# Kernel tuning notes

Measured on AMD Instinct MI355X. Metric: run time of the kernel, lower is better.

The kernel has to match this reference:

```python
import jax, jax.numpy as jnp
import numpy as np

N_NODES = 10000
N_EDGES = 640000
IN_FEATS = 256
H_FEATS = 128
NUM_CLASSES = 64


def _kaiming(key, shape):
    fan_in = shape[1]
    std = np.sqrt(2.0 / fan_in)
    return jax.random.normal(key, shape, dtype=jnp.float32) * std


def setup_inputs() -> dict:
    key = jax.random.key(0)
    ks = jax.random.split(key, 10)
    x = jax.random.normal(ks[0], (N_NODES, IN_FEATS), dtype=jnp.float32)
    edge_index = jax.random.randint(ks[1], (2, N_EDGES), 0, N_NODES, dtype=jnp.int64)
    return {
        "x": x,
        "edge_index": edge_index,
        "W_lin": _kaiming(ks[2], (H_FEATS, IN_FEATS)),
        "b_lin": jnp.zeros((H_FEATS,), jnp.float32),
        "Wl1": _kaiming(ks[3], (H_FEATS, H_FEATS)),
        "bl1": jnp.zeros((H_FEATS,), jnp.float32),
        "Wr1": _kaiming(ks[4], (H_FEATS, H_FEATS)),
        "Wl2": _kaiming(ks[5], (H_FEATS, H_FEATS)),
        "bl2": jnp.zeros((H_FEATS,), jnp.float32),
        "Wr2": _kaiming(ks[6], (H_FEATS, H_FEATS)),
        "W_cls": _kaiming(ks[7], (NUM_CLASSES, H_FEATS)),
    }


def _sage_conv(x, src, dst, Wl, bl, Wr, n_nodes):
    # PyG SAGEConv (mean aggr): out = lin_l(mean_{j->i} x_j) + lin_r(x_i)
    msg = x[src]                                    # [E, H] gather
    agg = jax.ops.segment_sum(msg, dst, num_segments=n_nodes)  # [N, H]
    deg = jax.ops.segment_sum(jnp.ones((src.shape[0],), x.dtype), dst,
                              num_segments=n_nodes)            # [N]
    mean = agg / jnp.maximum(deg, 1.0)[:, None]
    return mean @ Wl.T + bl + x @ Wr.T


def reference(x, edge_index, W_lin, b_lin, Wl1, bl1, Wr1, Wl2, bl2, Wr2, W_cls):
    src, dst = edge_index[0], edge_index[1]
    n = x.shape[0]
    h = jax.nn.relu(x @ W_lin.T + b_lin)            # input projection + relu
    h = _sage_conv(h, src, dst, Wl1, bl1, Wr1, n)   # sage1 (no relu: linear is truthy)
    h = _sage_conv(h, src, dst, Wl2, bl2, Wr2, n)   # sage2
    h = jax.nn.relu(h)
    return h @ W_cls.T                              # weight.mm(x.t()).t()
```

## Files before the change

kernel.cpp:

```cpp
#include <hip/hip_runtime.h>

#define NN 10000
#define HF 128
#define INF_ 256
#define CLS 64
#define CAP 128
#define RT  (NN / 16)

typedef __attribute__((ext_vector_type(8))) short short8;
typedef __attribute__((ext_vector_type(4))) float f32x4;

__device__ __forceinline__ unsigned short f2bf(float f) {
    unsigned u = __builtin_bit_cast(unsigned, f);
    u = (u + 0x7fffu + ((u >> 16) & 1u)) >> 16;
    return (unsigned short)u;
}
__device__ __forceinline__ float bfbits2f(unsigned u) {
    u <<= 16;
    return __builtin_bit_cast(float, u);
}


template <int K, int NC>
__device__ __forceinline__
void mfma_cols(int row_tile, int col0,
               const unsigned short* __restrict__ A,
               const unsigned short* __restrict__ W, f32x4* acc) {
    int lane = threadIdx.x & 63;
    int m = lane & 15, quad = lane >> 4;
    const short8* ap = (const short8*)(A + (size_t)(row_tile * 16 + m) * K + quad * 8);
    const short8* bp[NC];
#pragma unroll
    for (int c = 0; c < NC; ++c)
        bp[c] = (const short8*)(W + (size_t)(col0 + c * 16 + m) * K + quad * 8);
#pragma unroll
    for (int k0 = 0; k0 < K; k0 += 32) {
        int ki = k0 >> 3;
        short8 a = ap[ki];
#pragma unroll
        for (int c = 0; c < NC; ++c)
            acc[c] = __builtin_amdgcn_mfma_f32_16x16x32_bf16(a, bp[c][ki], acc[c], 0, 0, 0);
    }
}

template <int NC, bool OUT_BF16, bool RELU_OUT, bool HAS_BIAS, bool HAS_TMP>
__device__ __forceinline__
void epilogue_n(int row_tile, int col0, int N, const float* __restrict__ bias,
                const float* __restrict__ tmp, f32x4* acc, void* __restrict__ out) {
    int lane = threadIdx.x & 63;
    int m = lane & 15, quad = lane >> 4;
#pragma unroll
    for (int c = 0; c < NC; ++c) {
        int colg = col0 + c * 16 + m;
        float bv = HAS_BIAS ? bias[colg] : 0.f;
#pragma unroll
        for (int r = 0; r < 4; ++r) {
            int rowg = row_tile * 16 + quad * 4 + r;
            float v = acc[c][r] + bv;
            if (HAS_TMP) v += tmp[(size_t)rowg * N + colg];
            if (RELU_OUT) v = fmaxf(v, 0.f);
            if (OUT_BF16) ((unsigned short*)out)[(size_t)rowg * N + colg] = f2bf(v);
            else          ((float*)out)[(size_t)rowg * N + colg] = v;
        }
    }
}

__device__ __forceinline__ short8 pack8(float4 a, float4 b) {
    short8 r;
    r[0] = (short)f2bf(a.x); r[1] = (short)f2bf(a.y);
    r[2] = (short)f2bf(a.z); r[3] = (short)f2bf(a.w);
    r[4] = (short)f2bf(b.x); r[5] = (short)f2bf(b.y);
    r[6] = (short)f2bf(b.z); r[7] = (short)f2bf(b.w);
    return r;
}

__device__ __forceinline__
void gemm1_wave(int row_tile, int col0, const float* __restrict__ x,
                const float* __restrict__ Wlin, const float* __restrict__ blin,
                unsigned short* __restrict__ h0) {
    int lane = threadIdx.x & 63;
    int m = lane & 15, quad = lane >> 4;
    const float* ar = x    + (size_t)(row_tile * 16 + m) * INF_ + quad * 8;
    const float* w0 = Wlin + (size_t)(col0 +  0 + m) * INF_ + quad * 8;
    const float* w1 = Wlin + (size_t)(col0 + 16 + m) * INF_ + quad * 8;
    const float* w2 = Wlin + (size_t)(col0 + 32 + m) * INF_ + quad * 8;
    const float* w3 = Wlin + (size_t)(col0 + 48 + m) * INF_ + quad * 8;
    f32x4 acc[4] = {};
#pragma unroll
    for (int k0 = 0; k0 < INF_; k0 += 32) {
        short8 a  = pack8(*(const float4*)(ar + k0), *(const float4*)(ar + k0 + 4));
        short8 b0 = pack8(*(const float4*)(w0 + k0), *(const float4*)(w0 + k0 + 4));
        short8 b1 = pack8(*(const float4*)(w1 + k0), *(const float4*)(w1 + k0 + 4));
        short8 b2 = pack8(*(const float4*)(w2 + k0), *(const float4*)(w2 + k0 + 4));
        short8 b3 = pack8(*(const float4*)(w3 + k0), *(const float4*)(w3 + k0 + 4));
        acc[0] = __builtin_amdgcn_mfma_f32_16x16x32_bf16(a, b0, acc[0], 0, 0, 0);
        acc[1] = __builtin_amdgcn_mfma_f32_16x16x32_bf16(a, b1, acc[1], 0, 0, 0);
        acc[2] = __builtin_amdgcn_mfma_f32_16x16x32_bf16(a, b2, acc[2], 0, 0, 0);
        acc[3] = __builtin_amdgcn_mfma_f32_16x16x32_bf16(a, b3, acc[3], 0, 0, 0);
    }
    epilogue_n<4, true, true, true, false>(row_tile, col0, HF, blin, nullptr, acc, h0);
}

#define GB 313
#define FB 2500
#define CB 288

__global__ __launch_bounds__(256)
void fused_k(const float* __restrict__ x, const float* __restrict__ Wlin,
             const float* __restrict__ blin, unsigned short* __restrict__ h0,
             const int* __restrict__ src, const int* __restrict__ dst,
             int* __restrict__ cnt, unsigned short* __restrict__ colb, int E,
             const float* __restrict__ Wl1, const float* __restrict__ Wr1,
             const float* __restrict__ Wl2, const float* __restrict__ Wr2,
             const float* __restrict__ Wcls, unsigned short* __restrict__ wb) {
    int b = blockIdx.x;
    if (b < GB) {
        int wave = threadIdx.x >> 6;
        int row_tile = b * 2 + (wave >> 1);
        if (row_tile >= RT) return;
        gemm1_wave(row_tile, (wave & 1) * 64, x, Wlin, blin, h0);
    } else if (b < GB + FB) {
        int i = (b - GB) * 256 + threadIdx.x;
        if (i < E) {
            int d = dst[i];
            int pos = atomicAdd(&cnt[d], 1);
            if (pos < CAP) colb[(size_t)d * CAP + pos] = (unsigned short)src[i];
        }
    } else {
        int i = (b - GB - FB) * 256 + threadIdx.x;
        const float* s; int off;
        if      (i < 16384) { s = Wl1;  off = 0; }
        else if (i < 32768) { s = Wr1;  off = 16384; }
        else if (i < 49152) { s = Wl2;  off = 32768; }
        else if (i < 65536) { s = Wr2;  off = 49152; }
        else if (i < 73728) { s = Wcls; off = 65536; }
        else return;
        wb[i] = f2bf(s[i - off]);
    }
}

#define AGB 2500

__global__ __launch_bounds__(256)
void agg_gemm_k(const unsigned short* __restrict__ h, const int* __restrict__ cnt,
                const unsigned short* __restrict__ colb, unsigned short* __restrict__ mv,
                const unsigned short* __restrict__ Wr, float* __restrict__ tmp, int n) {
    int b = blockIdx.x;
    if (b < AGB) {
        int wave = threadIdx.x >> 6;
        int lane = threadIdx.x & 63;
        int q   = lane >> 4;
        int r16 = lane & 15;
        int node = b * 4 + wave;
        if (node >= n) return;
        int deg = cnt[node];
        int c = deg > CAP ? CAP : deg;
        const unsigned short* mycol = colb + (size_t)node * CAP;
        const uint4* __restrict__ hp = (const uint4*)h;

        float a0 = 0.f, a1 = 0.f, a2 = 0.f, a3 = 0.f;
        float a4 = 0.f, a5 = 0.f, a6 = 0.f, a7 = 0.f;
        for (int base = 0; base < c; base += 64) {
            int mm = min(64, c - base);
            int colv = (base + lane < c) ? (int)mycol[base + lane] : 0;
#pragma unroll 4
            for (int jj = 0; jj < 16; ++jj) {
                if (jj * 4 >= mm) break;
                int e = jj * 4 + q;
                int s = __shfl(colv, e);
                if (e < mm) {
                    uint4 v = hp[(size_t)s * 16 + r16];
                    a0 += bfbits2f(v.x & 0xffffu); a1 += bfbits2f(v.x >> 16);
                    a2 += bfbits2f(v.y & 0xffffu); a3 += bfbits2f(v.y >> 16);
                    a4 += bfbits2f(v.z & 0xffffu); a5 += bfbits2f(v.z >> 16);
                    a6 += bfbits2f(v.w & 0xffffu); a7 += bfbits2f(v.w >> 16);
                }
            }
        }
        a0 += __shfl_xor(a0, 16); a0 += __shfl_xor(a0, 32);
        a1 += __shfl_xor(a1, 16); a1 += __shfl_xor(a1, 32);
        a2 += __shfl_xor(a2, 16); a2 += __shfl_xor(a2, 32);
        a3 += __shfl_xor(a3, 16); a3 += __shfl_xor(a3, 32);
        a4 += __shfl_xor(a4, 16); a4 += __shfl_xor(a4, 32);
        a5 += __shfl_xor(a5, 16); a5 += __shfl_xor(a5, 32);
        a6 += __shfl_xor(a6, 16); a6 += __shfl_xor(a6, 32);
        a7 += __shfl_xor(a7, 16); a7 += __shfl_xor(a7, 32);
        if (q == 0) {
            float inv = (deg > 0) ? 1.0f / (float)deg : 0.f;
            uint4 o;
            o.x = (unsigned)f2bf(a0 * inv) | ((unsigned)f2bf(a1 * inv) << 16);
            o.y = (unsigned)f2bf(a2 * inv) | ((unsigned)f2bf(a3 * inv) << 16);
            o.z = (unsigned)f2bf(a4 * inv) | ((unsigned)f2bf(a5 * inv) << 16);
            o.w = (unsigned)f2bf(a6 * inv) | ((unsigned)f2bf(a7 * inv) << 16);
            ((uint4*)mv)[(size_t)node * 16 + r16] = o;
        }
    } else {
        int bb = b - AGB;
        int wave = threadIdx.x >> 6;
        int row_tile = bb * 2 + (wave >> 1);
        if (row_tile >= RT) return;
        int col0 = (wave & 1) * 64;
        f32x4 acc[4] = {};
        mfma_cols<HF, 4>(row_tile, col0, h, Wr, acc);
        epilogue_n<4, false, false, false, false>(row_tile, col0, HF,
                                                  nullptr, nullptr, acc, tmp);
    }
}

__global__ __launch_bounds__(256)
void sage_fin_k(const unsigned short* __restrict__ mv, const unsigned short* __restrict__ Wl,
                const float* __restrict__ tmp, const float* __restrict__ bias,
                unsigned short* __restrict__ out) {
    int wave = threadIdx.x >> 6;
    int row_tile = blockIdx.x * 2 + (wave >> 1);
    if (row_tile >= RT) return;
    int col0 = (wave & 1) * 64;
    f32x4 acc[4] = {};
    mfma_cols<HF, 4>(row_tile, col0, mv, Wl, acc);
    epilogue_n<4, true, false, true, true>(row_tile, col0, HF, bias, tmp, acc, out);
}

__global__ __launch_bounds__(256)
void fin2_cls_k(const unsigned short* __restrict__ mv, const unsigned short* __restrict__ Wl,
                const float* __restrict__ tmp, const float* __restrict__ bias,
                const unsigned short* __restrict__ Wc, float* __restrict__ out) {
    __shared__ unsigned short h2s[2][16][HF];
    int wave = threadIdx.x >> 6;
    int lane = threadIdx.x & 63;
    int m = lane & 15, quad = lane >> 4;

    int t1 = wave >> 1;
    int rt1 = blockIdx.x * 2 + t1;
    if (rt1 >= RT) rt1 = RT - 1;
    int col0 = (wave & 1) * 64;
    f32x4 acc[4] = {};
    mfma_cols<HF, 4>(rt1, col0, mv, Wl, acc);
#pragma unroll
    for (int c = 0; c < 4; ++c) {
        int colg = col0 + c * 16 + m;
        float bv = bias[colg];
#pragma unroll
        for (int r = 0; r < 4; ++r) {
            int rl = quad * 4 + r;
            float v = acc[c][r] + bv + tmp[(size_t)(rt1 * 16 + rl) * HF + colg];
            h2s[t1][rl][colg] = f2bf(fmaxf(v, 0.f));
        }
    }
    __syncthreads();

    int t2 = wave >> 1;
    int rt2 = blockIdx.x * 2 + t2;
    if (rt2 >= RT) rt2 = RT - 1;
    int cc0 = (wave & 1) * 32;
    const unsigned short* As = &h2s[t2][0][0];
    f32x4 cacc[2] = {};
    mfma_cols<HF, 2>(0, cc0, As, Wc, cacc);
    epilogue_n<2, false, false, false, false>(0, 0, 0, nullptr, nullptr, cacc, nullptr);
#pragma unroll
    for (int c = 0; c < 2; ++c) {
        int colg = cc0 + c * 16 + m;
#pragma unroll
        for (int r = 0; r < 4; ++r) {
            int rowg = rt2 * 16 + quad * 4 + r;
            out[(size_t)rowg * CLS + colg] = cacc[c][r];
        }
    }
}


extern "C" void kernel_launch(void* const* d_in, const int* in_sizes, int n_in,
                              void* d_out, int out_size, void* d_ws, size_t ws_size,
                              hipStream_t stream) {
    const float* x      = (const float*)d_in[0];
    const int*   ei     = (const int*)d_in[1];
    const float* W_lin  = (const float*)d_in[2];
    const float* b_lin  = (const float*)d_in[3];
    const float* Wl1    = (const float*)d_in[4];
    const float* bl1    = (const float*)d_in[5];
    const float* Wr1    = (const float*)d_in[6];
    const float* Wl2    = (const float*)d_in[7];
    const float* bl2    = (const float*)d_in[8];
    const float* Wr2    = (const float*)d_in[9];
    const float* W_cls  = (const float*)d_in[10];
    float* out = (float*)d_out;

    const int E = in_sizes[1] / 2;
    const int* src = ei;
    const int* dst = ei + E;

    unsigned short* wb  = (unsigned short*)d_ws;
    unsigned short* wbl1 = wb;
    unsigned short* wbr1 = wb + 16384;
    unsigned short* wbl2 = wb + 32768;
    unsigned short* wbr2 = wb + 49152;
    unsigned short* wbc  = wb + 65536;
    unsigned short* h0  = wb + 73728;
    unsigned short* mv  = h0 + (size_t)NN * HF;
    unsigned short* h1  = mv + (size_t)NN * HF;
    float* tmp = (float*)(h1 + (size_t)NN * HF);
    int* cnt = (int*)(tmp + (size_t)NN * HF);
    unsigned short* colb = (unsigned short*)(cnt + NN);

    hipMemsetAsync(cnt, 0, NN * sizeof(int), stream);

    fused_k<<<GB + FB + CB, 256, 0, stream>>>(
        x, W_lin, b_lin, h0, src, dst, cnt, colb, E,
        Wl1, Wr1, Wl2, Wr2, W_cls, wb);

    agg_gemm_k<<<AGB + 313, 256, 0, stream>>>(h0, cnt, colb, mv, wbr1, tmp, NN);
    sage_fin_k<<<313, 256, 0, stream>>>(mv, wbl1, tmp, bl1, h1);

    agg_gemm_k<<<AGB + 313, 256, 0, stream>>>(h1, cnt, colb, mv, wbr2, tmp, NN);
    fin2_cls_k<<<313, 256, 0, stream>>>(mv, wbl2, tmp, bl2, wbc, out);
}
```

Before: 181.4 us.

## Fuse neighbor aggregation with SAGE GEMMs per 16-node tile in LDS

Each SAGE layer's gather-mean, root GEMM, neighbor GEMM and epilogue now run in one kernel. A 1024-thread block handles 16 nodes, one wave per node, and stages the mean rows in padded LDS. The second layer also fuses the ReLU and classifier GEMM. This drops two launches per forward and the global round-trips of the mean and fp32 temporary buffers. In exchange, blocks are large (625 blocks of 1024 threads) and only 8 of 16 waves do the MFMA work, so occupancy and load balance may suffer.

```diff
diff --git a/kernel.cpp b/kernel.cpp
--- a/kernel.cpp
+++ b/kernel.cpp
@@ -6,6 +6,7 @@
 #define CLS 64
 #define CAP 128
 #define RT  (NN / 16)
+#define LDP (HF + 8)
 
 typedef __attribute__((ext_vector_type(8))) short short8;
 typedef __attribute__((ext_vector_type(4))) float f32x4;
@@ -24,22 +25,21 @@
 template <int K, int NC>
 __device__ __forceinline__
 void mfma_cols(int row_tile, int col0,
-               const unsigned short* __restrict__ A,
+               const unsigned short* __restrict__ A, int lda,
                const unsigned short* __restrict__ W, f32x4* acc) {
     int lane = threadIdx.x & 63;
     int m = lane & 15, quad = lane >> 4;
-    const short8* ap = (const short8*)(A + (size_t)(row_tile * 16 + m) * K + quad * 8);
+    const unsigned short* arow = A + (size_t)(row_tile * 16 + m) * lda + quad * 8;
     const short8* bp[NC];
 #pragma unroll
     for (int c = 0; c < NC; ++c)
         bp[c] = (const short8*)(W + (size_t)(col0 + c * 16 + m) * K + quad * 8);
 #pragma unroll
     for (int k0 = 0; k0 < K; k0 += 32) {
-        int ki = k0 >> 3;
-        short8 a = ap[ki];
+        short8 a = *(const short8*)(arow + k0);
 #pragma unroll
         for (int c = 0; c < NC; ++c)
-            acc[c] = __builtin_amdgcn_mfma_f32_16x16x32_bf16(a, bp[c][ki], acc[c], 0, 0, 0);
+            acc[c] = __builtin_amdgcn_mfma_f32_16x16x32_bf16(a, bp[c][k0 >> 3], acc[c], 0, 0, 0);
     }
 }
 
@@ -139,131 +139,109 @@
     }
 }
 
-#define AGB 2500
-
-__global__ __launch_bounds__(256)
-void agg_gemm_k(const unsigned short* __restrict__ h, const int* __restrict__ cnt,
-                const unsigned short* __restrict__ colb, unsigned short* __restrict__ mv,
-                const unsigned short* __restrict__ Wr, float* __restrict__ tmp, int n) {
-    int b = blockIdx.x;
-    if (b < AGB) {
-        int wave = threadIdx.x >> 6;
-        int lane = threadIdx.x & 63;
-        int q   = lane >> 4;
-        int r16 = lane & 15;
-        int node = b * 4 + wave;
-        if (node >= n) return;
-        int deg = cnt[node];
-        int c = deg > CAP ? CAP : deg;
-        const unsigned short* mycol = colb + (size_t)node * CAP;
-        const uint4* __restrict__ hp = (const uint4*)h;
-
-        float a0 = 0.f, a1 = 0.f, a2 = 0.f, a3 = 0.f;
-        float a4 = 0.f, a5 = 0.f, a6 = 0.f, a7 = 0.f;
-        for (int base = 0; base < c; base += 64) {
-            int mm = min(64, c - base);
-            int colv = (base + lane < c) ? (int)mycol[base + lane] : 0;
+__device__ __forceinline__
+void gather_mean(const unsigned short* __restrict__ h, int deg,
+                 const unsigned short* __restrict__ mycol,
+                 unsigned short* __restrict__ msrow) {
+    int lane = threadIdx.x & 63;
+    int q   = lane >> 4;
+    int r16 = lane & 15;
+    int c = deg > CAP ? CAP : deg;
+    const uint4* __restrict__ hp = (const uint4*)h;
+
+    float a0 = 0.f, a1 = 0.f, a2 = 0.f, a3 = 0.f;
+    float a4 = 0.f, a5 = 0.f, a6 = 0.f, a7 = 0.f;
+    for (int base = 0; base < c; base += 64) {
+        int mm = min(64, c - base);
+        int colv = (base + lane < c) ? (int)mycol[base + lane] : 0;
 #pragma unroll 4
-            for (int jj = 0; jj < 16; ++jj) {
-                if (jj * 4 >= mm) break;
-                int e = jj * 4 + q;
-                int s = __shfl(colv, e);
-                if (e < mm) {
-                    uint4 v = hp[(size_t)s * 16 + r16];
-                    a0 += bfbits2f(v.x & 0xffffu); a1 += bfbits2f(v.x >> 16);
-                    a2 += bfbits2f(v.y & 0xffffu); a3 += bfbits2f(v.y >> 16);
-                    a4 += bfbits2f(v.z & 0xffffu); a5 += bfbits2f(v.z >> 16);
-                    a6 += bfbits2f(v.w & 0xffffu); a7 += bfbits2f(v.w >> 16);
-                }
+        for (int jj = 0; jj < 16; ++jj) {
+            if (jj * 4 >= mm) break;
+            int e = jj * 4 + q;
+            int s = __shfl(colv, e);
+            if (e < mm) {
+                uint4 v = hp[(size_t)s * 16 + r16];
+                a0 += bfbits2f(v.x & 0xffffu); a1 += bfbits2f(v.x >> 16);
+                a2 += bfbits2f(v.y & 0xffffu); a3 += bfbits2f(v.y >> 16);
+                a4 += bfbits2f(v.z & 0xffffu); a5 += bfbits2f(v.z >> 16);
+                a6 += bfbits2f(v.w & 0xffffu); a7 += bfbits2f(v.w >> 16);
             }
         }
-        a0 += __shfl_xor(a0, 16); a0 += __shfl_xor(a0, 32);
-        a1 += __shfl_xor(a1, 16); a1 += __shfl_xor(a1, 32);
-        a2 += __shfl_xor(a2, 16); a2 += __shfl_xor(a2, 32);
-        a3 += __shfl_xor(a3, 16); a3 += __shfl_xor(a3, 32);
-        a4 += __shfl_xor(a4, 16); a4 += __shfl_xor(a4, 32);
-        a5 += __shfl_xor(a5, 16); a5 += __shfl_xor(a5, 32);
-        a6 += __shfl_xor(a6, 16); a6 += __shfl_xor(a6, 32);
-        a7 += __shfl_xor(a7, 16); a7 += __shfl_xor(a7, 32);
-        if (q == 0) {
-            float inv = (deg > 0) ? 1.0f / (float)deg : 0.f;
-            uint4 o;
-            o.x = (unsigned)f2bf(a0 * inv) | ((unsigned)f2bf(a1 * inv) << 16);
-            o.y = (unsigned)f2bf(a2 * inv) | ((unsigned)f2bf(a3 * inv) << 16);
-            o.z = (unsigned)f2bf(a4 * inv) | ((unsigned)f2bf(a5 * inv) << 16);
-            o.w = (unsigned)f2bf(a6 * inv) | ((unsigned)f2bf(a7 * inv) << 16);
-            ((uint4*)mv)[(size_t)node * 16 + r16] = o;
-        }
-    } else {
-        int bb = b - AGB;
-        int wave = threadIdx.x >> 6;
-        int row_tile = bb * 2 + (wave >> 1);
-        if (row_tile >= RT) return;
-        int col0 = (wave & 1) * 64;
-        f32x4 acc[4] = {};
-        mfma_cols<HF, 4>(row_tile, col0, h, Wr, acc);
-        epilogue_n<4, false, false, false, false>(row_tile, col0, HF,
-                                                  nullptr, nullptr, acc, tmp);
-    }
-}
-
-__global__ __launch_bounds__(256)
-void sage_fin_k(const unsigned short* __restrict__ mv, const unsigned short* __restrict__ Wl,
-                const float* __restrict__ tmp, const float* __restrict__ bias,
-                unsigned short* __restrict__ out) {
+    }
+    a0 += __shfl_xor(a0, 16); a0 += __shfl_xor(a0, 32);
+    a1 += __shfl_xor(a1, 16); a1 += __shfl_xor(a1, 32);
+    a2 += __shfl_xor(a2, 16); a2 += __shfl_xor(a2, 32);
+    a3 += __shfl_xor(a3, 16); a3 += __shfl_xor(a3, 32);
+    a4 += __shfl_xor(a4, 16); a4 += __shfl_xor(a4, 32);
+    a5 += __shfl_xor(a5, 16); a5 += __shfl_xor(a5, 32);
+    a6 += __shfl_xor(a6, 16); a6 += __shfl_xor(a6, 32);
+    a7 += __shfl_xor(a7, 16); a7 += __shfl_xor(a7, 32);
+    if (q == 0) {
+        float inv = (deg > 0) ? 1.0f / (float)deg : 0.f;
+        uint4 o;
+        o.x = (unsigned)f2bf(a0 * inv) | ((unsigned)f2bf(a1 * inv) << 16);
+        o.y = (unsigned)f2bf(a2 * inv) | ((unsigned)f2bf(a3 * inv) << 16);
+        o.z = (unsigned)f2bf(a4 * inv) | ((unsigned)f2bf(a5 * inv) << 16);
+        o.w = (unsigned)f2bf(a6 * inv) | ((unsigned)f2bf(a7 * inv) << 16);
+        ((uint4*)msrow)[r16] = o;
+    }
+}
+
+__global__ __launch_bounds__(1024)
+void aggfin1_k(const unsigned short* __restrict__ h0, const int* __restrict__ cnt,
+               const unsigned short* __restrict__ colb,
+               const unsigned short* __restrict__ Wr, const unsigned short* __restrict__ Wl,
+               const float* __restrict__ bias, unsigned short* __restrict__ h1) {
+    __shared__ __align__(16) unsigned short ms[16][LDP];
     int wave = threadIdx.x >> 6;
-    int row_tile = blockIdx.x * 2 + (wave >> 1);
-    if (row_tile >= RT) return;
-    int col0 = (wave & 1) * 64;
-    f32x4 acc[4] = {};
-    mfma_cols<HF, 4>(row_tile, col0, mv, Wl, acc);
-    epilogue_n<4, true, false, true, true>(row_tile, col0, HF, bias, tmp, acc, out);
-}
-
-__global__ __launch_bounds__(256)
-void fin2_cls_k(const unsigned short* __restrict__ mv, const unsigned short* __restrict__ Wl,
-                const float* __restrict__ tmp, const float* __restrict__ bias,
-                const unsigned short* __restrict__ Wc, float* __restrict__ out) {
-    __shared__ unsigned short h2s[2][16][HF];
+    int node = blockIdx.x * 16 + wave;
+    gather_mean(h0, cnt[node], colb + (size_t)node * CAP, &ms[wave][0]);
+
+    f32x4 acc[1] = {};
+    if (wave < 8)
+        mfma_cols<HF, 1>(blockIdx.x, wave * 16, h0, HF, Wr, acc);
+    __syncthreads();
+    if (wave < 8) {
+        mfma_cols<HF, 1>(0, wave * 16, &ms[0][0], LDP, Wl, acc);
+        epilogue_n<1, true, false, true, false>(blockIdx.x, wave * 16, HF,
+                                                bias, nullptr, acc, h1);
+    }
+}
+
+__global__ __launch_bounds__(1024)
+void aggfin2cls_k(const unsigned short* __restrict__ h1, const int* __restrict__ cnt,
+                  const unsigned short* __restrict__ colb,
+                  const unsigned short* __restrict__ Wr, const unsigned short* __restrict__ Wl,
+                  const float* __restrict__ bias, const unsigned short* __restrict__ Wc,
+                  float* __restrict__ out) {
+    __shared__ __align__(16) unsigned short ms[16][LDP];
+    __shared__ __align__(16) unsigned short h2s[16][LDP];
     int wave = threadIdx.x >> 6;
     int lane = threadIdx.x & 63;
     int m = lane & 15, quad = lane >> 4;
-
-    int t1 = wave >> 1;
-    int rt1 = blockIdx.x * 2 + t1;
-    if (rt1 >= RT) rt1 = RT - 1;
-    int col0 = (wave & 1) * 64;
-    f32x4 acc[4] = {};
-    mfma_cols<HF, 4>(rt1, col0, mv, Wl, acc);
-#pragma unroll
-    for (int c = 0; c < 4; ++c) {
-        int colg = col0 + c * 16 + m;
+    int node = blockIdx.x * 16 + wave;
+    gather_mean(h1, cnt[node], colb + (size_t)node * CAP, &ms[wave][0]);
+
+    f32x4 acc[1] = {};
+    if (wave < 8)
+        mfma_cols<HF, 1>(blockIdx.x, wave * 16, h1, HF, Wr, acc);
+    __syncthreads();
+    if (wave < 8) {
+        mfma_cols<HF, 1>(0, wave * 16, &ms[0][0], LDP, Wl, acc);
+        int colg = wave * 16 + m;
         float bv = bias[colg];
 #pragma unroll
         for (int r = 0; r < 4; ++r) {
-            int rl = quad * 4 + r;
-            float v = acc[c][r] + bv + tmp[(size_t)(rt1 * 16 + rl) * HF + colg];
-            h2s[t1][rl][colg] = f2bf(fmaxf(v, 0.f));
+            float v = acc[0][r] + bv;
+            h2s[quad * 4 + r][colg] = f2bf(fmaxf(v, 0.f));
         }
     }
     __syncthreads();
-
-    int t2 = wave >> 1;
-    int rt2 = blockIdx.x * 2 + t2;
-    if (rt2 >= RT) rt2 = RT - 1;
-    int cc0 = (wave & 1) * 32;
-    const unsigned short* As = &h2s[t2][0][0];
-    f32x4 cacc[2] = {};
-    mfma_cols<HF, 2>(0, cc0, As, Wc, cacc);
-    epilogue_n<2, false, false, false, false>(0, 0, 0, nullptr, nullptr, cacc, nullptr);
-#pragma unroll
-    for (int c = 0; c < 2; ++c) {
-        int colg = cc0 + c * 16 + m;
-#pragma unroll
-        for (int r = 0; r < 4; ++r) {
-            int rowg = rt2 * 16 + quad * 4 + r;
-            out[(size_t)rowg * CLS + colg] = cacc[c][r];
-        }
+    if (wave < 4) {
+        f32x4 cacc[1] = {};
+        mfma_cols<HF, 1>(0, wave * 16, &h2s[0][0], LDP, Wc, cacc);
+        epilogue_n<1, false, false, false, false>(blockIdx.x, wave * 16, CLS,
+                                                  nullptr, nullptr, cacc, out);
     }
 }
 
@@ -295,10 +273,8 @@
     unsigned short* wbr2 = wb + 49152;
     unsigned short* wbc  = wb + 65536;
     unsigned short* h0  = wb + 73728;
-    unsigned short* mv  = h0 + (size_t)NN * HF;
-    unsigned short* h1  = mv + (size_t)NN * HF;
-    float* tmp = (float*)(h1 + (size_t)NN * HF);
-    int* cnt = (int*)(tmp + (size_t)NN * HF);
+    unsigned short* h1  = h0 + (size_t)NN * HF;
+    int* cnt = (int*)(h1 + (size_t)NN * HF);
     unsigned short* colb = (unsigned short*)(cnt + NN);
 
     hipMemsetAsync(cnt, 0, NN * sizeof(int), stream);
@@ -307,9 +283,7 @@
         x, W_lin, b_lin, h0, src, dst, cnt, colb, E,
         Wl1, Wr1, Wl2, Wr2, W_cls, wb);
 
-    agg_gemm_k<<<AGB + 313, 256, 0, stream>>>(h0, cnt, colb, mv, wbr1, tmp, NN);
-    sage_fin_k<<<313, 256, 0, stream>>>(mv, wbl1, tmp, bl1, h1);
-
-    agg_gemm_k<<<AGB + 313, 256, 0, stream>>>(h1, cnt, colb, mv, wbr2, tmp, NN);
-    fin2_cls_k<<<313, 256, 0, stream>>>(mv, wbl2, tmp, bl2, wbc, out);
-}
+    aggfin1_k<<<RT, 1024, 0, stream>>>(h0, cnt, colb, wbr1, wbl1, bl1, h1);
+
+    aggfin2cls_k<<<RT, 1024, 0, stream>>>(h1, cnt, colb, wbr2, wbl2, bl2, wbc, out);
+}
```

New measurement: 170.0 us. -6.2%, faster.
